# Kernel tuning notes

Measured on AMD Instinct MI355X. Metric: run time of the kernel, lower is better.

## Reference

```python
import jax, jax.numpy as jnp
import numpy as np

PRIMES = (2, 3, 5, 7, 11, 13, 17, 19, 23, 29)
TEMP = 1000.0  # softmax_temperature
B, S = 32, 2048

def _templates(p):
    # circle template for residue r: (cos(2*pi*r/p), sin(2*pi*r/p)) -> [p, 2]
    ang = 2.0 * np.pi * np.arange(p) / p
    return jnp.asarray(np.stack([np.cos(ang), np.sin(ang)], axis=-1).astype(np.float32))

def _mul_onehot(p):
    # onehot[a, b, (a*b) % p] = 1 -> [p, p, p]
    t = (np.arange(p)[:, None] * np.arange(p)[None, :]) % p
    return jnp.asarray((t[..., None] == np.arange(p)).astype(np.float32))

TEMPLATES = [_templates(p) for p in PRIMES]
MUL_OH = [_mul_onehot(p) for p in PRIMES]

def setup_inputs() -> dict:
    key = jax.random.key(0)
    k1, k2 = jax.random.split(key)
    m = len(PRIMES)
    return {
        "a_circle": jax.random.normal(k1, (B, S, m, 2), dtype=jnp.float32),
        "b_circle": jax.random.normal(k2, (B, S, m, 2), dtype=jnp.float32),
    }

def _circle_add(a, b):
    # complex multiply: angles add -> (a + b) mod p on the circle
    ca, sa = a[..., 0], a[..., 1]
    cb, sb = b[..., 0], b[..., 1]
    return jnp.stack([ca * cb - sa * sb, sa * cb + ca * sb], axis=-1)

def _circle_sub(a, b):
    # a - b = a + conj(b): negate sin of b
    b_conj = jnp.stack([b[..., 0], -b[..., 1]], axis=-1)
    return _circle_add(a, b_conj)

def _decode_soft(c_i, tmpl):
    # c_i: [B, S, 2], tmpl: [p, 2] -> soft one-hot over residues [B, S, p]
    sim = jnp.einsum('bsd,pd->bsp', c_i, tmpl)
    return jax.nn.softmax(TEMP * sim, axis=-1)

def _circle_mul(a, b):
    outs = []
    for i, p in enumerate(PRIMES):
        tmpl = TEMPLATES[i]
        a_soft = _decode_soft(a[:, :, i, :], tmpl)
        b_soft = _decode_soft(b[:, :, i, :], tmpl)
        # outer product of soft residues contracted with mul table
        dist = jnp.einsum('bsi,bsj,ijk->bsk', a_soft, b_soft, MUL_OH[i])
        outs.append(dist @ tmpl)  # re-encode to circle: [B, S, 2]
    return jnp.stack(outs, axis=2)  # [B, S, m, 2]

def reference(a_circle, b_circle):
    add = _circle_add(a_circle, b_circle)
    sub = _circle_sub(a_circle, b_circle)
    mul = _circle_mul(a_circle, b_circle)
    return jnp.stack([add, sub, mul], axis=0)  # [3, B, S, m, 2]
```

## Files before the change

### kernel.cpp

```cpp
#include <hip/hip_runtime.h>


#define TEMP_LOG2E 1442.6950408889634f

constexpr double PI_D = 3.14159265358979323846264338327950288;

constexpr double tay_cos(double x) {
    double x2 = x * x, term = 1.0, sum = 1.0;
    for (int k = 1; k <= 15; ++k) { term *= -x2 / double((2 * k - 1) * (2 * k)); sum += term; }
    return sum;
}
constexpr double tay_sin(double x) {
    double x2 = x * x, term = x, sum = x;
    for (int k = 1; k <= 15; ++k) { term *= -x2 / double((2 * k) * (2 * k + 1)); sum += term; }
    return sum;
}
constexpr double ang_red(int r, int P) {
    double x = 2.0 * PI_D * double(r) / double(P);
    return (x > PI_D) ? x - 2.0 * PI_D : x;
}

template <int P> struct TabS { float c[P]; float s[P]; };
template <int P>
constexpr TabS<P> make_tabs() {
    TabS<P> t{};
    for (int r = 0; r < P; ++r) {
        t.c[r] = (float)(double(TEMP_LOG2E) * tay_cos(ang_red(r, P)));
        t.s[r] = (float)(double(TEMP_LOG2E) * tay_sin(ang_red(r, P)));
    }
    return t;
}
template <int P> struct TabE { float c[P / 2 + 1]; float s[P / 2 + 1]; };
template <int P>
constexpr TabE<P> make_tabe() {
    TabE<P> t{};
    for (int k = 0; k <= P / 2; ++k) {
        t.c[k] = (float)tay_cos(ang_red(k, P));
        t.s[k] = (float)tay_sin(ang_red(k, P));
    }
    return t;
}

template <int P>
__device__ __forceinline__ void mul_prime(float ca, float sa, float cb, float sb,
                                          float& oc, float& os) {
    static_assert(P % 2 == 1, "generic path requires odd P");
    constexpr int H = (P - 1) / 2;
    constexpr TabS<P> T = make_tabs<P>();
    constexpr TabE<P> E = make_tabe<P>();

    float ma = -1e30f, mb = -1e30f;
#pragma unroll
    for (int r = 0; r < P; ++r) {
        ma = fmaxf(ma, ca * T.c[r] + sa * T.s[r]);
        mb = fmaxf(mb, cb * T.c[r] + sb * T.s[r]);
    }

    float eb0 = __builtin_amdgcn_exp2f(cb * T.c[0] - mb);
    float Sb = eb0;
    float ub[H], vb[H];
#pragma unroll
    for (int j = 1; j <= H; ++j) {
        float e1 = __builtin_amdgcn_exp2f(cb * T.c[j] + sb * T.s[j] - mb);
        float e2 = __builtin_amdgcn_exp2f(cb * T.c[P - j] + sb * T.s[P - j] - mb);
        Sb += e1 + e2;
        ub[j - 1] = e1 + e2;
        vb[j - 1] = e1 - e2;
    }

    float A[H], Bacc[H];
#pragma unroll
    for (int k = 0; k < H; ++k) { A[k] = 0.f; Bacc[k] = 0.f; }

    float ea0 = __builtin_amdgcn_exp2f(ca * T.c[0] - ma);
    float Sa = ea0;
#pragma unroll
    for (int i = 1; i <= H; ++i) {
        float f1 = __builtin_amdgcn_exp2f(ca * T.c[i] + sa * T.s[i] - ma);
        float f2 = __builtin_amdgcn_exp2f(ca * T.c[P - i] + sa * T.s[P - i] - ma);
        Sa += f1 + f2;
        const float ua = f1 + f2, va = f1 - f2;
#pragma unroll
        for (int j = 1; j <= H; ++j) {
            const int k0 = (i * j) % P;
            const int kr = (k0 <= H) ? k0 : P - k0;
            A[kr - 1] = fmaf(ua, ub[j - 1], A[kr - 1]);
            if (k0 <= H) Bacc[kr - 1] = fmaf(va,  vb[j - 1], Bacc[kr - 1]);
            else         Bacc[kr - 1] = fmaf(-va, vb[j - 1], Bacc[kr - 1]);
        }
    }

    const float W0 = ea0 * Sb + eb0 * (Sa - ea0);

    float accC = W0, accS = 0.f;
#pragma unroll
    for (int k = 1; k <= H; ++k) {
        accC = fmaf(A[k - 1],    E.c[k], accC);
        accS = fmaf(Bacc[k - 1], E.s[k], accS);
    }
    const float inv = 1.0f / (Sa * Sb);
    oc = accC * inv;
    os = accS * inv;
}

template <>
__device__ __forceinline__ void mul_prime<2>(float ca, float sa, float cb, float sb,
                                             float& oc, float& os) {
    const float ka = ca * TEMP_LOG2E, kb = cb * TEMP_LOG2E;
    const float ma = fabsf(ka), mb = fabsf(kb);
    const float ea0 = __builtin_amdgcn_exp2f(ka - ma);
    const float ea1 = __builtin_amdgcn_exp2f(-ka - ma);
    const float eb0 = __builtin_amdgcn_exp2f(kb - mb);
    const float eb1 = __builtin_amdgcn_exp2f(-kb - mb);
    const float Sa = ea0 + ea1, Sb = eb0 + eb1;
    const float W0 = ea0 * Sb + eb0 * Sa - ea0 * eb0;
    const float W1 = ea1 * eb1;
    oc = (W0 - W1) / (Sa * Sb);
    os = 0.f;
}

__global__ __launch_bounds__(256, 2) void arith_kernel(const float* __restrict__ a,
                                                       const float* __restrict__ b,
                                                       float* __restrict__ out,
                                                       int n_pairs) {
    __shared__ float2 ta[128 * 11], tb[128 * 11], om[128 * 11];

    const int t = threadIdx.x;
    const int gbase = blockIdx.x * 1280;
    const int planef2 = n_pairs * 10;
    float2* o = (float2*)out;

#pragma unroll
    for (int it = 0; it < 5; ++it) {
        const int idx = it * 256 + t;
        const int pr = idx / 10, of = idx - pr * 10;
        const int sl = pr * 11 + of;
        const float2 av = ((const float2*)a)[gbase + idx];
        const float2 bv = ((const float2*)b)[gbase + idx];
        ta[sl] = av;
        tb[sl] = bv;
        const float pcc = av.x * bv.x, pss = av.y * bv.y;
        const float psc = av.y * bv.x, pcs = av.x * bv.y;
        o[gbase + idx]            = make_float2(pcc - pss, psc + pcs);
        o[planef2 + gbase + idx]  = make_float2(pcc + pss, psc - pcs);
    }
    __syncthreads();

    {
        const int lane = t & 63;
        const int row = ((t >> 6) & 1) * 64 + lane;
        const int rb = row * 11;

#define DO_PRIME(P, OFI)                                                     \
        {                                                                    \
            const float2 av = ta[rb + (OFI)];                                \
            const float2 bv = tb[rb + (OFI)];                                \
            float oc, os;                                                    \
            mul_prime<P>(av.x, av.y, bv.x, bv.y, oc, os);                    \
            om[rb + (OFI)] = make_float2(oc, os);                            \
        }

        if (t < 128) {
            DO_PRIME(29, 9)
            DO_PRIME(17, 6)
            DO_PRIME(13, 5)
            DO_PRIME(2, 0)
        } else {
            DO_PRIME(23, 8)
            DO_PRIME(19, 7)
            DO_PRIME(11, 4)
            DO_PRIME(7, 3)
            DO_PRIME(5, 2)
            DO_PRIME(3, 1)
        }
#undef DO_PRIME
    }
    __syncthreads();

#pragma unroll
    for (int it = 0; it < 5; ++it) {
        const int idx = it * 256 + t;
        const int pr = idx / 10, of = idx - pr * 10;
        o[2 * planef2 + gbase + idx] = om[pr * 11 + of];
    }
}

extern "C" void kernel_launch(void* const* d_in, const int* in_sizes, int n_in,
                              void* d_out, int out_size, void* d_ws, size_t ws_size,
                              hipStream_t stream) {
    const float* a = (const float*)d_in[0];
    const float* b = (const float*)d_in[1];
    float* out = (float*)d_out;
    const int n_pairs = in_sizes[0] / 20;
    const int n_blocks = n_pairs / 128;

    dim3 block(256);
    dim3 grid(n_blocks);
    arith_kernel<<<grid, block, 0, stream>>>(a, b, out, n_pairs);
}
```

Measured before the change: 70.79 us.

## Halve block size, vectorize global IO to float4, and fold softmax templates

The kernel now uses 128-thread blocks handling 64 pairs, and loads and stores with float4 for most of the tile, plus a float2 tail. The mul result overwrites the input shared buffer instead of using a separate one, which cuts LDS use. The per-prime math is rewritten with compile-time index sequences: symmetric templates share the c*cos term across the max and exp steps, and the max/subtract is folded into FMAs. The division is replaced by a hardware reciprocal, which may lose a little precision.

```diff
diff --git a/kernel.cpp b/kernel.cpp
--- a/kernel.cpp
+++ b/kernel.cpp
@@ -20,25 +20,100 @@
     return (x > PI_D) ? x - 2.0 * PI_D : x;
 }
 
-template <int P> struct TabS { float c[P]; float s[P]; };
+template <int... Is> struct iseq {};
+template <int N, int... Is> struct mkseq : mkseq<N - 1, N - 1, Is...> {};
+template <int... Is> struct mkseq<0, Is...> { using type = iseq<Is...>; };
+template <int N> using iseq_t = typename mkseq<N>::type;
+
+template <int P, int R> struct CS {
+    static constexpr float tc = (float)(double(TEMP_LOG2E) * tay_cos(ang_red(R, P)));
+    static constexpr float ts = (float)(double(TEMP_LOG2E) * tay_sin(ang_red(R, P)));
+    static constexpr float ec = (float)tay_cos(ang_red(R, P));
+    static constexpr float es = (float)tay_sin(ang_red(R, P));
+};
+
+template <int P, int J>
+__device__ __forceinline__ void smax_step(float c, float s, float& m0, float& m1) {
+    const float u = c * CS<P, J>::tc;
+    const float w = s * CS<P, J>::ts;
+    m0 = fmaxf(m0, u + w);
+    m1 = fmaxf(m1, u - w);
+}
+template <int P, int... J>
+__device__ __forceinline__ float smax_impl(float c, float s, iseq<J...>) {
+    float m0 = c * CS<P, 0>::tc;
+    float m1 = -3.0e38f;
+    (smax_step<P, J + 1>(c, s, m0, m1), ...);
+    return fmaxf(m0, m1);
+}
 template <int P>
-constexpr TabS<P> make_tabs() {
-    TabS<P> t{};
-    for (int r = 0; r < P; ++r) {
-        t.c[r] = (float)(double(TEMP_LOG2E) * tay_cos(ang_red(r, P)));
-        t.s[r] = (float)(double(TEMP_LOG2E) * tay_sin(ang_red(r, P)));
-    }
-    return t;
-}
-template <int P> struct TabE { float c[P / 2 + 1]; float s[P / 2 + 1]; };
-template <int P>
-constexpr TabE<P> make_tabe() {
-    TabE<P> t{};
-    for (int k = 0; k <= P / 2; ++k) {
-        t.c[k] = (float)tay_cos(ang_red(k, P));
-        t.s[k] = (float)tay_sin(ang_red(k, P));
-    }
-    return t;
+__device__ __forceinline__ float simmax(float c, float s) {
+    return smax_impl<P>(c, s, iseq_t<(P - 1) / 2>{});
+}
+
+template <int P, int J, int H>
+__device__ __forceinline__ void b_step(float cb, float sb, float nmb, float& Sb,
+                                       float (&ub)[H], float (&vb)[H]) {
+    const float u = fmaf(cb, CS<P, J>::tc, nmb);
+    const float w = sb * CS<P, J>::ts;
+    const float e1 = __builtin_amdgcn_exp2f(u + w);
+    const float e2 = __builtin_amdgcn_exp2f(u - w);
+    const float uu = e1 + e2;
+    Sb += uu;
+    ub[J - 1] = uu;
+    vb[J - 1] = e1 - e2;
+}
+template <int P, int H, int... J>
+__device__ __forceinline__ void b_fold(float cb, float sb, float nmb, float& Sb,
+                                       float (&ub)[H], float (&vb)[H], iseq<J...>) {
+    (b_step<P, J + 1, H>(cb, sb, nmb, Sb, ub, vb), ...);
+}
+
+template <int P, int I, int J, int H>
+__device__ __forceinline__ void pair_step(float ua, float va,
+                                          const float (&ub)[H], const float (&vb)[H],
+                                          float (&A)[H], float (&B)[H]) {
+    constexpr int K0 = (I * J) % P;
+    constexpr int KR = (K0 <= H) ? K0 : P - K0;
+    A[KR - 1] = fmaf(ua, ub[J - 1], A[KR - 1]);
+    if constexpr (K0 <= H) B[KR - 1] = fmaf(va,  vb[J - 1], B[KR - 1]);
+    else                   B[KR - 1] = fmaf(-va, vb[J - 1], B[KR - 1]);
+}
+template <int P, int I, int H, int... J>
+__device__ __forceinline__ void pair_row(float ua, float va,
+                                         const float (&ub)[H], const float (&vb)[H],
+                                         float (&A)[H], float (&B)[H], iseq<J...>) {
+    (pair_step<P, I, J + 1, H>(ua, va, ub, vb, A, B), ...);
+}
+template <int P, int I, int H>
+__device__ __forceinline__ void a_step(float ca, float sa, float nma, float& Sa,
+                                       const float (&ub)[H], const float (&vb)[H],
+                                       float (&A)[H], float (&B)[H]) {
+    const float u = fmaf(ca, CS<P, I>::tc, nma);
+    const float w = sa * CS<P, I>::ts;
+    const float f1 = __builtin_amdgcn_exp2f(u + w);
+    const float f2 = __builtin_amdgcn_exp2f(u - w);
+    const float ua = f1 + f2, va = f1 - f2;
+    Sa += ua;
+    pair_row<P, I, H>(ua, va, ub, vb, A, B, iseq_t<H>{});
+}
+template <int P, int H, int... I>
+__device__ __forceinline__ void a_fold(float ca, float sa, float nma, float& Sa,
+                                       const float (&ub)[H], const float (&vb)[H],
+                                       float (&A)[H], float (&B)[H], iseq<I...>) {
+    (a_step<P, I + 1, H>(ca, sa, nma, Sa, ub, vb, A, B), ...);
+}
+
+template <int P, int K, int H>
+__device__ __forceinline__ void enc_step(const float (&A)[H], const float (&B)[H],
+                                         float& accC, float& accS) {
+    accC = fmaf(A[K - 1], CS<P, K>::ec, accC);
+    accS = fmaf(B[K - 1], CS<P, K>::es, accS);
+}
+template <int P, int H, int... K>
+__device__ __forceinline__ void enc_fold(const float (&A)[H], const float (&B)[H],
+                                         float& accC, float& accS, iseq<K...>) {
+    (enc_step<P, K + 1, H>(A, B, accC, accS), ...);
 }
 
 template <int P>
@@ -46,59 +121,26 @@
                                           float& oc, float& os) {
     static_assert(P % 2 == 1, "generic path requires odd P");
     constexpr int H = (P - 1) / 2;
-    constexpr TabS<P> T = make_tabs<P>();
-    constexpr TabE<P> E = make_tabe<P>();
-
-    float ma = -1e30f, mb = -1e30f;
-#pragma unroll
-    for (int r = 0; r < P; ++r) {
-        ma = fmaxf(ma, ca * T.c[r] + sa * T.s[r]);
-        mb = fmaxf(mb, cb * T.c[r] + sb * T.s[r]);
-    }
-
-    float eb0 = __builtin_amdgcn_exp2f(cb * T.c[0] - mb);
+
+    const float nma = -simmax<P>(ca, sa);
+    const float nmb = -simmax<P>(cb, sb);
+
+    const float eb0 = __builtin_amdgcn_exp2f(fmaf(cb, CS<P, 0>::tc, nmb));
+    float ub[H], vb[H];
     float Sb = eb0;
-    float ub[H], vb[H];
-#pragma unroll
-    for (int j = 1; j <= H; ++j) {
-        float e1 = __builtin_amdgcn_exp2f(cb * T.c[j] + sb * T.s[j] - mb);
-        float e2 = __builtin_amdgcn_exp2f(cb * T.c[P - j] + sb * T.s[P - j] - mb);
-        Sb += e1 + e2;
-        ub[j - 1] = e1 + e2;
-        vb[j - 1] = e1 - e2;
-    }
-
-    float A[H], Bacc[H];
-#pragma unroll
-    for (int k = 0; k < H; ++k) { A[k] = 0.f; Bacc[k] = 0.f; }
-
-    float ea0 = __builtin_amdgcn_exp2f(ca * T.c[0] - ma);
+    b_fold<P, H>(cb, sb, nmb, Sb, ub, vb, iseq_t<H>{});
+
+    float A[H] = {}, B[H] = {};
+    const float ea0 = __builtin_amdgcn_exp2f(fmaf(ca, CS<P, 0>::tc, nma));
     float Sa = ea0;
-#pragma unroll
-    for (int i = 1; i <= H; ++i) {
-        float f1 = __builtin_amdgcn_exp2f(ca * T.c[i] + sa * T.s[i] - ma);
-        float f2 = __builtin_amdgcn_exp2f(ca * T.c[P - i] + sa * T.s[P - i] - ma);
-        Sa += f1 + f2;
-        const float ua = f1 + f2, va = f1 - f2;
-#pragma unroll
-        for (int j = 1; j <= H; ++j) {
-            const int k0 = (i * j) % P;
-            const int kr = (k0 <= H) ? k0 : P - k0;
-            A[kr - 1] = fmaf(ua, ub[j - 1], A[kr - 1]);
-            if (k0 <= H) Bacc[kr - 1] = fmaf(va,  vb[j - 1], Bacc[kr - 1]);
-            else         Bacc[kr - 1] = fmaf(-va, vb[j - 1], Bacc[kr - 1]);
-        }
-    }
+    a_fold<P, H>(ca, sa, nma, Sa, ub, vb, A, B, iseq_t<H>{});
 
     const float W0 = ea0 * Sb + eb0 * (Sa - ea0);
 
     float accC = W0, accS = 0.f;
-#pragma unroll
-    for (int k = 1; k <= H; ++k) {
-        accC = fmaf(A[k - 1],    E.c[k], accC);
-        accS = fmaf(Bacc[k - 1], E.s[k], accS);
-    }
-    const float inv = 1.0f / (Sa * Sb);
+    enc_fold<P, H>(A, B, accC, accS, iseq_t<H>{});
+
+    const float inv = __builtin_amdgcn_rcpf(Sa * Sb);
     oc = accC * inv;
     os = accS * inv;
 }
@@ -115,41 +157,63 @@
     const float Sa = ea0 + ea1, Sb = eb0 + eb1;
     const float W0 = ea0 * Sb + eb0 * Sa - ea0 * eb0;
     const float W1 = ea1 * eb1;
-    oc = (W0 - W1) / (Sa * Sb);
+    const float inv = __builtin_amdgcn_rcpf(Sa * Sb);
+    oc = (W0 - W1) * inv;
     os = 0.f;
 }
 
-__global__ __launch_bounds__(256, 2) void arith_kernel(const float* __restrict__ a,
+__global__ __launch_bounds__(128, 4) void arith_kernel(const float* __restrict__ a,
                                                        const float* __restrict__ b,
                                                        float* __restrict__ out,
                                                        int n_pairs) {
-    __shared__ float2 ta[128 * 11], tb[128 * 11], om[128 * 11];
+    __shared__ float2 ta[64 * 11], tb[64 * 11];
 
     const int t = threadIdx.x;
-    const int gbase = blockIdx.x * 1280;
+    const int gb2 = blockIdx.x * 640;
+    const int gb4 = blockIdx.x * 320;
     const int planef2 = n_pairs * 10;
-    float2* o = (float2*)out;
+    const int planef4 = planef2 >> 1;
+    float2* o2 = (float2*)out;
+    float4* o4 = (float4*)out;
+    const float4* a4 = (const float4*)a;
+    const float4* b4 = (const float4*)b;
 
 #pragma unroll
-    for (int it = 0; it < 5; ++it) {
-        const int idx = it * 256 + t;
-        const int pr = idx / 10, of = idx - pr * 10;
+    for (int it = 0; it < 2; ++it) {
+        const int k = it * 128 + t;
+        const int pr = k / 5, j = k - pr * 5;
+        const int sl = pr * 11 + 2 * j;
+        const float4 av = a4[gb4 + k];
+        const float4 bv = b4[gb4 + k];
+        ta[sl]     = make_float2(av.x, av.y);
+        ta[sl + 1] = make_float2(av.z, av.w);
+        tb[sl]     = make_float2(bv.x, bv.y);
+        tb[sl + 1] = make_float2(bv.z, bv.w);
+        float4 addv, subv;
+        addv.x = av.x * bv.x - av.y * bv.y;  addv.y = av.y * bv.x + av.x * bv.y;
+        addv.z = av.z * bv.z - av.w * bv.w;  addv.w = av.w * bv.z + av.z * bv.w;
+        subv.x = av.x * bv.x + av.y * bv.y;  subv.y = av.y * bv.x - av.x * bv.y;
+        subv.z = av.z * bv.z + av.w * bv.w;  subv.w = av.w * bv.z - av.z * bv.w;
+        o4[gb4 + k]           = addv;
+        o4[planef4 + gb4 + k] = subv;
+    }
+    {
+        const int f2 = 512 + t;
+        const int pr = f2 / 10, of = f2 - pr * 10;
         const int sl = pr * 11 + of;
-        const float2 av = ((const float2*)a)[gbase + idx];
-        const float2 bv = ((const float2*)b)[gbase + idx];
+        const float2 av = ((const float2*)a)[gb2 + f2];
+        const float2 bv = ((const float2*)b)[gb2 + f2];
         ta[sl] = av;
         tb[sl] = bv;
         const float pcc = av.x * bv.x, pss = av.y * bv.y;
         const float psc = av.y * bv.x, pcs = av.x * bv.y;
-        o[gbase + idx]            = make_float2(pcc - pss, psc + pcs);
-        o[planef2 + gbase + idx]  = make_float2(pcc + pss, psc - pcs);
+        o2[gb2 + f2]            = make_float2(pcc - pss, psc + pcs);
+        o2[planef2 + gb2 + f2]  = make_float2(pcc + pss, psc - pcs);
     }
     __syncthreads();
 
     {
-        const int lane = t & 63;
-        const int row = ((t >> 6) & 1) * 64 + lane;
-        const int rb = row * 11;
+        const int rb = (t & 63) * 11;
 
 #define DO_PRIME(P, OFI)                                                     \
         {                                                                    \
@@ -157,10 +221,10 @@
             const float2 bv = tb[rb + (OFI)];                                \
             float oc, os;                                                    \
             mul_prime<P>(av.x, av.y, bv.x, bv.y, oc, os);                    \
-            om[rb + (OFI)] = make_float2(oc, os);                            \
+            ta[rb + (OFI)] = make_float2(oc, os);                            \
         }
 
-        if (t < 128) {
+        if (t < 64) {
             DO_PRIME(29, 9)
             DO_PRIME(17, 6)
             DO_PRIME(13, 5)
@@ -178,10 +242,17 @@
     __syncthreads();
 
 #pragma unroll
-    for (int it = 0; it < 5; ++it) {
-        const int idx = it * 256 + t;
-        const int pr = idx / 10, of = idx - pr * 10;
-        o[2 * planef2 + gbase + idx] = om[pr * 11 + of];
+    for (int it = 0; it < 2; ++it) {
+        const int k = it * 128 + t;
+        const int pr = k / 5, j = k - pr * 5;
+        const int sl = pr * 11 + 2 * j;
+        const float2 r0 = ta[sl], r1 = ta[sl + 1];
+        o4[2 * planef4 + gb4 + k] = make_float4(r0.x, r0.y, r1.x, r1.y);
+    }
+    {
+        const int f2 = 512 + t;
+        const int pr = f2 / 10, of = f2 - pr * 10;
+        o2[2 * planef2 + gb2 + f2] = ta[pr * 11 + of];
     }
 }
 
@@ -192,9 +263,9 @@
     const float* b = (const float*)d_in[1];
     float* out = (float*)d_out;
     const int n_pairs = in_sizes[0] / 20;
-    const int n_blocks = n_pairs / 128;
-
-    dim3 block(256);
+    const int n_blocks = n_pairs / 64;
+
+    dim3 block(128);
     dim3 grid(n_blocks);
     arith_kernel<<<grid, block, 0, stream>>>(a, b, out, n_pairs);
 }
```

Result: no change. 70.66 us (-0.2%).
